# Kernel tuning notes

Hardware: AMD Instinct MI355X
Metric: run time of the kernel (lower is better)

The kernel has to match this reference:

```python
import jax, jax.numpy as jnp
import numpy as np

N_NODES = 100000
N_EDGES = 1600000
IN_DIM = 128
OUT_DIM = 256
EPS = 1e-12


def setup_inputs() -> dict:
    key = jax.random.key(0)
    k1, k2, k3, k4, k5 = jax.random.split(key, 5)
    x = jax.random.normal(k1, (N_NODES, IN_DIM), dtype=jnp.float32)
    edge_index = jax.random.randint(k2, (2, N_EDGES), 0, N_NODES, dtype=jnp.int64)
    edge_weight = jax.random.uniform(k3, (N_EDGES,), dtype=jnp.float32)
    # nn.Linear(in_dim*2, out_dim): weight [out, 2*in], bias [out]
    bound = 1.0 / np.sqrt(2 * IN_DIM)
    W = jax.random.uniform(k4, (OUT_DIM, 2 * IN_DIM), minval=-bound, maxval=bound, dtype=jnp.float32)
    b = jax.random.uniform(k5, (OUT_DIM,), minval=-bound, maxval=bound, dtype=jnp.float32)
    return {"x": x, "edge_index": edge_index, "edge_weight": edge_weight, "W": W, "b": b}


def reference(x, edge_index, edge_weight, W, b):
    src = edge_index[0]
    dst = edge_index[1]
    w = edge_weight.astype(x.dtype)
    # messages: [E, in_dim] = gathered dst features weighted per-edge
    messages = x[dst] * w[:, None]
    agg = jax.ops.segment_sum(messages, src, num_segments=x.shape[0])   # [N, in_dim]
    wsum = jax.ops.segment_sum(w, src, num_segments=x.shape[0])        # [N]
    neigh = agg / jnp.maximum(wsum, EPS)[:, None]
    h = jnp.concatenate([x, neigh], axis=1)                            # [N, 2*in_dim]
    h = h @ W.T + b
    return jax.nn.relu(h)  # dropout is identity in eval / p=0.0
```

## Files before the change

kernel.cpp:

```cpp
#include <hip/hip_runtime.h>
#include <hip/hip_bf16.h>

#define IN_DIM 128
#define OUT_DIM 256
#define KDIM 256
#define EPS 1e-12f
#define CB_NODES 128
#define NB_MAX 1024
#define PART_CHUNK 8192
#define CAP 2560

typedef __attribute__((ext_vector_type(8))) short short8;
typedef __attribute__((ext_vector_type(4))) float f32x4;

static __device__ __forceinline__ unsigned short f2bf(float f) {
  __hip_bfloat16 h = __float2bfloat16(f);
  return *reinterpret_cast<unsigned short*>(&h);
}
static __device__ __forceinline__ unsigned pack2bf(float a, float b) {
  return (unsigned)f2bf(a) | ((unsigned)f2bf(b) << 16);
}
static __device__ __forceinline__ float bf_lo(unsigned v) {
  return __uint_as_float((v & 0xffffu) << 16);
}
static __device__ __forceinline__ float bf_hi(unsigned v) {
  return __uint_as_float(v & 0xffff0000u);
}

__global__ __launch_bounds__(256) void cvt_x(
    const float* __restrict__ x, unsigned short* __restrict__ hb, int N) {
  const int total = N * 32;
  const int stride = gridDim.x * blockDim.x;
  for (int idx = blockIdx.x * blockDim.x + threadIdx.x; idx < total; idx += stride) {
    const int row = idx >> 5;
    const int c4 = (idx & 31) * 4;
    const float4 v = *reinterpret_cast<const float4*>(x + (size_t)row * IN_DIM + c4);
    ushort4 o;
    o.x = f2bf(v.x); o.y = f2bf(v.y); o.z = f2bf(v.z); o.w = f2bf(v.w);
    *reinterpret_cast<ushort4*>(hb + (size_t)row * KDIM + c4) = o;
  }
}

__global__ __launch_bounds__(256) void chist(
    const int* __restrict__ src, int* __restrict__ cnt, int E, int NB) {
  __shared__ int lcnt[NB_MAX];
  for (int i = threadIdx.x; i < NB; i += 256) lcnt[i] = 0;
  __syncthreads();
  const int stride = gridDim.x * blockDim.x;
  for (int e = blockIdx.x * blockDim.x + threadIdx.x; e < E; e += stride)
    atomicAdd(&lcnt[src[e] >> 7], 1);
  __syncthreads();
  for (int i = threadIdx.x; i < NB; i += 256)
    if (lcnt[i]) atomicAdd(&cnt[i], lcnt[i]);
}

__global__ void cscan(const int* __restrict__ cnt, int* __restrict__ bstart,
                      int* __restrict__ gcursor, int NB) {
  const int lane = threadIdx.x;
  int carry = 0;
  for (int base = 0; base < NB; base += 64) {
    const int i = base + lane;
    const int c = (i < NB) ? cnt[i] : 0;
    int incl = c;
    for (int d = 1; d < 64; d <<= 1) {
      int t = __shfl_up(incl, d, 64);
      if (lane >= d) incl += t;
    }
    const int excl = carry + incl - c;
    if (i < NB) { bstart[i] = excl; gcursor[i] = excl; }
    carry += __shfl(incl, 63, 64);
  }
  if (lane == 0) bstart[NB] = carry;
}

__global__ __launch_bounds__(256) void cpartition(
    const int* __restrict__ src, const int* __restrict__ dst,
    const float* __restrict__ ew,
    int* __restrict__ gcursor, int2* __restrict__ recs, int E, int NB) {
  __shared__ int pos[NB_MAX];
  const int c0 = blockIdx.x * PART_CHUNK;
  const int c1 = min(E, c0 + PART_CHUNK);
  for (int i = threadIdx.x; i < NB; i += 256) pos[i] = 0;
  __syncthreads();
  for (int i = c0 + threadIdx.x; i < c1; i += 256)
    atomicAdd(&pos[src[i] >> 7], 1);
  __syncthreads();
  for (int b = threadIdx.x; b < NB; b += 256) {
    const int c = pos[b];
    pos[b] = c ? atomicAdd(&gcursor[b], c) : 0;
  }
  __syncthreads();
  for (int i = c0 + threadIdx.x; i < c1; i += 256) {
    const int s = src[i];
    const int p = atomicAdd(&pos[s >> 7], 1);
    int2 r;
    r.x = dst[i] | ((s & 127) << 17);
    r.y = __float_as_int(ew[i]);
    recs[p] = r;
  }
}

__global__ __launch_bounds__(512) void cagg(
    unsigned short* __restrict__ hb,
    const int* __restrict__ bstart,
    const int2* __restrict__ recs, int N) {
  __shared__ int2 lrec[CAP];
  __shared__ int lstart[CB_NODES + 1];
  __shared__ int lcur[CB_NODES];
  const int tid = threadIdx.x;
  const int lane = tid & 63;
  const int wv = tid >> 6;
  const int blk = blockIdx.x;
  const int e0 = bstart[blk];
  const int e1 = bstart[blk + 1];

  float ax[16], ay[16], ws[16];
#pragma unroll
  for (int n = 0; n < 16; ++n) { ax[n] = 0.f; ay[n] = 0.f; ws[n] = 0.f; }

  for (int base = e0; base < e1; base += CAP) {
    const int m = min(CAP, e1 - base);
    if (tid < CB_NODES) lcur[tid] = 0;
    __syncthreads();
    for (int i = tid; i < m; i += 512)
      atomicAdd(&lcur[recs[base + i].x >> 17], 1);
    __syncthreads();
    if (wv == 0) {
      int carry = 0;
#pragma unroll
      for (int rr = 0; rr < 2; ++rr) {
        const int idx = rr * 64 + lane;
        const int c = lcur[idx];
        int incl = c;
#pragma unroll
        for (int d = 1; d < 64; d <<= 1) {
          int t = __shfl_up(incl, d, 64);
          if (lane >= d) incl += t;
        }
        lstart[idx] = carry + incl - c;
        carry += __shfl(incl, 63, 64);
      }
      if (lane == 0) lstart[CB_NODES] = carry;
    }
    __syncthreads();
    if (tid < CB_NODES) lcur[tid] = lstart[tid];
    __syncthreads();
    for (int i = tid; i < m; i += 512) {
      const int2 r = recs[base + i];
      const int p = atomicAdd(&lcur[r.x >> 17], 1);
      lrec[p] = r;
    }
    __syncthreads();
#pragma unroll
    for (int n = 0; n < 16; ++n) {
      const int rs = lstart[wv * 16 + n];
      const int re = lstart[wv * 16 + n + 1];
      int j = rs;
      for (; j + 4 <= re; j += 4) {
        const int2 r0 = lrec[j + 0];
        const int2 r1 = lrec[j + 1];
        const int2 r2 = lrec[j + 2];
        const int2 r3 = lrec[j + 3];
        const unsigned v0 = *reinterpret_cast<const unsigned*>(
            hb + (size_t)(r0.x & 0x1FFFF) * KDIM + lane * 2);
        const unsigned v1 = *reinterpret_cast<const unsigned*>(
            hb + (size_t)(r1.x & 0x1FFFF) * KDIM + lane * 2);
        const unsigned v2 = *reinterpret_cast<const unsigned*>(
            hb + (size_t)(r2.x & 0x1FFFF) * KDIM + lane * 2);
        const unsigned v3 = *reinterpret_cast<const unsigned*>(
            hb + (size_t)(r3.x & 0x1FFFF) * KDIM + lane * 2);
        const float w0 = __int_as_float(r0.y);
        const float w1 = __int_as_float(r1.y);
        const float w2 = __int_as_float(r2.y);
        const float w3 = __int_as_float(r3.y);
        ax[n] += bf_lo(v0) * w0 + bf_lo(v1) * w1 + bf_lo(v2) * w2 + bf_lo(v3) * w3;
        ay[n] += bf_hi(v0) * w0 + bf_hi(v1) * w1 + bf_hi(v2) * w2 + bf_hi(v3) * w3;
        ws[n] += w0 + w1 + w2 + w3;
      }
      for (; j < re; ++j) {
        const int2 r = lrec[j];
        const unsigned v = *reinterpret_cast<const unsigned*>(
            hb + (size_t)(r.x & 0x1FFFF) * KDIM + lane * 2);
        const float w = __int_as_float(r.y);
        ax[n] += bf_lo(v) * w;
        ay[n] += bf_hi(v) * w;
        ws[n] += w;
      }
    }
    __syncthreads();
  }

#pragma unroll
  for (int n = 0; n < 16; ++n) {
    const int row = wv * 16 + n;
    const int node = blk * CB_NODES + row;
    if (node < N) {
      const float mm = fmaxf(ws[n], EPS);
      *reinterpret_cast<unsigned*>(hb + (size_t)node * KDIM + IN_DIM + lane * 2) =
          pack2bf(ax[n] / mm, ay[n] / mm);
    }
  }
}

__global__ __launch_bounds__(512, 2) void sage_gemm_mfma(
    const unsigned short* __restrict__ hb,
    const float* __restrict__ W,
    const float* __restrict__ bias,
    float* __restrict__ out, int N) {
  __shared__ unsigned short Wl[OUT_DIM * KDIM];
  const int tid = threadIdx.x;
  const int lane = tid & 63;
  const int wv = tid >> 6;

  char* wl = reinterpret_cast<char*>(Wl);
  for (int ch = tid; ch < OUT_DIM * KDIM / 8; ch += 512) {
    const int elem = ch * 8;
    const int j = elem >> 8;
    const int col = elem & 255;
    const float4 w0 = *reinterpret_cast<const float4*>(W + elem);
    const float4 w1 = *reinterpret_cast<const float4*>(W + elem + 4);
    uint4 o;
    o.x = pack2bf(w0.x, w0.y); o.y = pack2bf(w0.z, w0.w);
    o.z = pack2bf(w1.x, w1.y); o.w = pack2bf(w1.z, w1.w);
    const int byte = (j << 9) | ((col * 2) ^ ((j & 7) << 4));
    *reinterpret_cast<uint4*>(wl + byte) = o;
  }

  const int row0 = blockIdx.x * 256 + wv * 32;
  const int kc = (lane >> 4) * 8;
  const unsigned short* arow0 = hb + (size_t)(row0 + (lane & 15)) * KDIM + kc;
  const unsigned short* arow1 = arow0 + 16 * KDIM;
  short8 a0[8], a1[8];
#pragma unroll
  for (int kk = 0; kk < 8; ++kk) {
    a0[kk] = *reinterpret_cast<const short8*>(arow0 + kk * 32);
    a1[kk] = *reinterpret_cast<const short8*>(arow1 + kk * 32);
  }

  __syncthreads();

  f32x4 acc[2][16];
#pragma unroll
  for (int i = 0; i < 2; ++i)
#pragma unroll
    for (int j = 0; j < 16; ++j) acc[i][j] = (f32x4){0.f, 0.f, 0.f, 0.f};

  const int jrow = lane & 15;
  const int kb0 = kc * 2;
#pragma unroll
  for (int kk = 0; kk < 8; ++kk) {
    const int kbyte = kb0 + kk * 64;
#pragma unroll
    for (int ct = 0; ct < 16; ++ct) {
      const int j = ct * 16 + jrow;
      const short8 bf = *reinterpret_cast<const short8*>(
          wl + ((j << 9) | (kbyte ^ ((j & 7) << 4))));
      acc[0][ct] = __builtin_amdgcn_mfma_f32_16x16x32_bf16(a0[kk], bf, acc[0][ct], 0, 0, 0);
      acc[1][ct] = __builtin_amdgcn_mfma_f32_16x16x32_bf16(a1[kk], bf, acc[1][ct], 0, 0, 0);
    }
  }

  const int col = lane & 15;
  const int rquad = (lane >> 4) * 4;
#pragma unroll
  for (int ct = 0; ct < 16; ++ct) {
    const int j = ct * 16 + col;
    const float bj = bias[j];
#pragma unroll
    for (int rt = 0; rt < 2; ++rt) {
      const int rbase = row0 + rt * 16 + rquad;
      const f32x4 a = acc[rt][ct];
#pragma unroll
      for (int r = 0; r < 4; ++r) {
        const int row = rbase + r;
        if (row < N) out[(size_t)row * OUT_DIM + j] = fmaxf(a[r] + bj, 0.f);
      }
    }
  }
}

extern "C" void kernel_launch(void* const* d_in, const int* in_sizes, int n_in,
                              void* d_out, int out_size, void* d_ws, size_t ws_size,
                              hipStream_t stream) {
  const float* x  = (const float*)d_in[0];
  const int*   ei = (const int*)d_in[1];
  const float* ew = (const float*)d_in[2];
  const float* W  = (const float*)d_in[3];
  const float* b  = (const float*)d_in[4];
  float* out = (float*)d_out;

  const int N = in_sizes[0] / IN_DIM;
  const int E = in_sizes[2];
  const int* src = ei;
  const int* dst = ei + E;

  const int gemm_blocks = (N + 255) / 256;
  const int Mpad = gemm_blocks * 256;
  const int NB = (N + CB_NODES - 1) / CB_NODES;

  unsigned short* hb = (unsigned short*)d_ws;
  int2* recs   = (int2*)(hb + (size_t)Mpad * KDIM);
  int* cnt     = (int*)(recs + E);
  int* bstart  = cnt + NB_MAX;
  int* gcursor = bstart + NB_MAX + 1;

  hipMemsetAsync(cnt, 0, NB * sizeof(int), stream);

  cvt_x<<<2048, 256, 0, stream>>>(x, hb, N);
  chist<<<256, 256, 0, stream>>>(src, cnt, E, NB);
  cscan<<<1, 64, 0, stream>>>(cnt, bstart, gcursor, NB);
  cpartition<<<(E + PART_CHUNK - 1) / PART_CHUNK, 256, 0, stream>>>(
      src, dst, ew, gcursor, recs, E, NB);
  cagg<<<NB, 512, 0, stream>>>(hb, bstart, recs, N);
  sage_gemm_mfma<<<gemm_blocks, 512, 0, stream>>>(hb, W, b, out, N);
}
```

Baseline: 401.2 us.

## Split aggregation into single-pass fast path, pre-convert W, retune partition chunks

Aggregation now has two kernels. cagg_fast handles node blocks whose edge count fits in shared memory in a single pass, keeping one node's accumulators live at a time with an 8-way unrolled gather, and declares a higher occupancy target. cagg_slow keeps the old multi-pass path for oversized blocks. W is converted to bf16 once by a separate kernel so the GEMM blocks no longer each convert it. PART_CHUNK is reduced and the histogram grid is doubled for more parallelism, at the cost of one extra kernel launch plus a mostly empty slow-path launch.

```diff
diff --git a/kernel.cpp b/kernel.cpp
--- a/kernel.cpp
+++ b/kernel.cpp
@@ -7,7 +7,7 @@
 #define EPS 1e-12f
 #define CB_NODES 128
 #define NB_MAX 1024
-#define PART_CHUNK 8192
+#define PART_CHUNK 2048
 #define CAP 2560
 
 typedef __attribute__((ext_vector_type(8))) short short8;
@@ -41,6 +41,15 @@
   }
 }
 
+__global__ __launch_bounds__(256) void cvt_w(
+    const float* __restrict__ W, unsigned short* __restrict__ Wb) {
+  const int base = (blockIdx.x * blockDim.x + threadIdx.x) * 4;
+  const float4 v = *reinterpret_cast<const float4*>(W + base);
+  ushort4 o;
+  o.x = f2bf(v.x); o.y = f2bf(v.y); o.z = f2bf(v.z); o.w = f2bf(v.w);
+  *reinterpret_cast<ushort4*>(Wb + base) = o;
+}
+
 __global__ __launch_bounds__(256) void chist(
     const int* __restrict__ src, int* __restrict__ cnt, int E, int NB) {
   __shared__ int lcnt[NB_MAX];
@@ -100,7 +109,7 @@
   }
 }
 
-__global__ __launch_bounds__(512) void cagg(
+__global__ __launch_bounds__(512, 8) void cagg_fast(
     unsigned short* __restrict__ hb,
     const int* __restrict__ bstart,
     const int2* __restrict__ recs, int N) {
@@ -113,6 +122,114 @@
   const int blk = blockIdx.x;
   const int e0 = bstart[blk];
   const int e1 = bstart[blk + 1];
+  const int m = e1 - e0;
+  if (m > CAP) return;
+
+  if (tid < CB_NODES) lcur[tid] = 0;
+  __syncthreads();
+  for (int i = tid; i < m; i += 512)
+    atomicAdd(&lcur[recs[e0 + i].x >> 17], 1);
+  __syncthreads();
+  if (wv == 0) {
+    int carry = 0;
+#pragma unroll
+    for (int rr = 0; rr < 2; ++rr) {
+      const int idx = rr * 64 + lane;
+      const int c = lcur[idx];
+      int incl = c;
+#pragma unroll
+      for (int d = 1; d < 64; d <<= 1) {
+        int t = __shfl_up(incl, d, 64);
+        if (lane >= d) incl += t;
+      }
+      lstart[idx] = carry + incl - c;
+      carry += __shfl(incl, 63, 64);
+    }
+    if (lane == 0) lstart[CB_NODES] = carry;
+  }
+  __syncthreads();
+  if (tid < CB_NODES) lcur[tid] = lstart[tid];
+  __syncthreads();
+  for (int i = tid; i < m; i += 512) {
+    const int2 r = recs[e0 + i];
+    lrec[atomicAdd(&lcur[r.x >> 17], 1)] = r;
+  }
+  __syncthreads();
+
+  for (int n = 0; n < 16; ++n) {
+    const int rs = lstart[wv * 16 + n];
+    const int re = lstart[wv * 16 + n + 1];
+    float ax = 0.f, ay = 0.f, ws = 0.f;
+    int j = rs;
+    for (; j + 8 <= re; j += 8) {
+      const int2 r0 = lrec[j + 0];
+      const int2 r1 = lrec[j + 1];
+      const int2 r2 = lrec[j + 2];
+      const int2 r3 = lrec[j + 3];
+      const int2 r4 = lrec[j + 4];
+      const int2 r5 = lrec[j + 5];
+      const int2 r6 = lrec[j + 6];
+      const int2 r7 = lrec[j + 7];
+      const unsigned v0 = *reinterpret_cast<const unsigned*>(hb + (size_t)(r0.x & 0x1FFFF) * KDIM + lane * 2);
+      const unsigned v1 = *reinterpret_cast<const unsigned*>(hb + (size_t)(r1.x & 0x1FFFF) * KDIM + lane * 2);
+      const unsigned v2 = *reinterpret_cast<const unsigned*>(hb + (size_t)(r2.x & 0x1FFFF) * KDIM + lane * 2);
+      const unsigned v3 = *reinterpret_cast<const unsigned*>(hb + (size_t)(r3.x & 0x1FFFF) * KDIM + lane * 2);
+      const unsigned v4 = *reinterpret_cast<const unsigned*>(hb + (size_t)(r4.x & 0x1FFFF) * KDIM + lane * 2);
+      const unsigned v5 = *reinterpret_cast<const unsigned*>(hb + (size_t)(r5.x & 0x1FFFF) * KDIM + lane * 2);
+      const unsigned v6 = *reinterpret_cast<const unsigned*>(hb + (size_t)(r6.x & 0x1FFFF) * KDIM + lane * 2);
+      const unsigned v7 = *reinterpret_cast<const unsigned*>(hb + (size_t)(r7.x & 0x1FFFF) * KDIM + lane * 2);
+      const float w0 = __int_as_float(r0.y), w1 = __int_as_float(r1.y);
+      const float w2 = __int_as_float(r2.y), w3 = __int_as_float(r3.y);
+      const float w4 = __int_as_float(r4.y), w5 = __int_as_float(r5.y);
+      const float w6 = __int_as_float(r6.y), w7 = __int_as_float(r7.y);
+      ax += bf_lo(v0) * w0 + bf_lo(v1) * w1 + bf_lo(v2) * w2 + bf_lo(v3) * w3
+          + bf_lo(v4) * w4 + bf_lo(v5) * w5 + bf_lo(v6) * w6 + bf_lo(v7) * w7;
+      ay += bf_hi(v0) * w0 + bf_hi(v1) * w1 + bf_hi(v2) * w2 + bf_hi(v3) * w3
+          + bf_hi(v4) * w4 + bf_hi(v5) * w5 + bf_hi(v6) * w6 + bf_hi(v7) * w7;
+      ws += w0 + w1 + w2 + w3 + w4 + w5 + w6 + w7;
+    }
+    for (; j + 2 <= re; j += 2) {
+      const int2 r0 = lrec[j + 0];
+      const int2 r1 = lrec[j + 1];
+      const unsigned v0 = *reinterpret_cast<const unsigned*>(hb + (size_t)(r0.x & 0x1FFFF) * KDIM + lane * 2);
+      const unsigned v1 = *reinterpret_cast<const unsigned*>(hb + (size_t)(r1.x & 0x1FFFF) * KDIM + lane * 2);
+      const float w0 = __int_as_float(r0.y), w1 = __int_as_float(r1.y);
+      ax += bf_lo(v0) * w0 + bf_lo(v1) * w1;
+      ay += bf_hi(v0) * w0 + bf_hi(v1) * w1;
+      ws += w0 + w1;
+    }
+    if (j < re) {
+      const int2 r = lrec[j];
+      const unsigned v = *reinterpret_cast<const unsigned*>(hb + (size_t)(r.x & 0x1FFFF) * KDIM + lane * 2);
+      const float w = __int_as_float(r.y);
+      ax += bf_lo(v) * w;
+      ay += bf_hi(v) * w;
+      ws += w;
+    }
+    const int node = blk * CB_NODES + wv * 16 + n;
+    if (node < N) {
+      const float mm = fmaxf(ws, EPS);
+      *reinterpret_cast<unsigned*>(hb + (size_t)node * KDIM + IN_DIM + lane * 2) =
+          pack2bf(ax / mm, ay / mm);
+    }
+  }
+}
+
+__global__ __launch_bounds__(512) void cagg_slow(
+    unsigned short* __restrict__ hb,
+    const int* __restrict__ bstart,
+    const int2* __restrict__ recs, int N) {
+  const int blk = blockIdx.x;
+  const int e0 = bstart[blk];
+  const int e1 = bstart[blk + 1];
+  if (e1 - e0 <= CAP) return;
+
+  __shared__ int2 lrec[CAP];
+  __shared__ int lstart[CB_NODES + 1];
+  __shared__ int lcur[CB_NODES];
+  const int tid = threadIdx.x;
+  const int lane = tid & 63;
+  const int wv = tid >> 6;
 
   float ax[16], ay[16], ws[16];
 #pragma unroll
@@ -147,37 +264,14 @@
     __syncthreads();
     for (int i = tid; i < m; i += 512) {
       const int2 r = recs[base + i];
-      const int p = atomicAdd(&lcur[r.x >> 17], 1);
-      lrec[p] = r;
+      lrec[atomicAdd(&lcur[r.x >> 17], 1)] = r;
     }
     __syncthreads();
 #pragma unroll
     for (int n = 0; n < 16; ++n) {
       const int rs = lstart[wv * 16 + n];
       const int re = lstart[wv * 16 + n + 1];
-      int j = rs;
-      for (; j + 4 <= re; j += 4) {
-        const int2 r0 = lrec[j + 0];
-        const int2 r1 = lrec[j + 1];
-        const int2 r2 = lrec[j + 2];
-        const int2 r3 = lrec[j + 3];
-        const unsigned v0 = *reinterpret_cast<const unsigned*>(
-            hb + (size_t)(r0.x & 0x1FFFF) * KDIM + lane * 2);
-        const unsigned v1 = *reinterpret_cast<const unsigned*>(
-            hb + (size_t)(r1.x & 0x1FFFF) * KDIM + lane * 2);
-        const unsigned v2 = *reinterpret_cast<const unsigned*>(
-            hb + (size_t)(r2.x & 0x1FFFF) * KDIM + lane * 2);
-        const unsigned v3 = *reinterpret_cast<const unsigned*>(
-            hb + (size_t)(r3.x & 0x1FFFF) * KDIM + lane * 2);
-        const float w0 = __int_as_float(r0.y);
-        const float w1 = __int_as_float(r1.y);
-        const float w2 = __int_as_float(r2.y);
-        const float w3 = __int_as_float(r3.y);
-        ax[n] += bf_lo(v0) * w0 + bf_lo(v1) * w1 + bf_lo(v2) * w2 + bf_lo(v3) * w3;
-        ay[n] += bf_hi(v0) * w0 + bf_hi(v1) * w1 + bf_hi(v2) * w2 + bf_hi(v3) * w3;
-        ws[n] += w0 + w1 + w2 + w3;
-      }
-      for (; j < re; ++j) {
+      for (int j = rs; j < re; ++j) {
         const int2 r = lrec[j];
         const unsigned v = *reinterpret_cast<const unsigned*>(
             hb + (size_t)(r.x & 0x1FFFF) * KDIM + lane * 2);
@@ -192,8 +286,7 @@
 
 #pragma unroll
   for (int n = 0; n < 16; ++n) {
-    const int row = wv * 16 + n;
-    const int node = blk * CB_NODES + row;
+    const int node = blk * CB_NODES + wv * 16 + n;
     if (node < N) {
       const float mm = fmaxf(ws[n], EPS);
       *reinterpret_cast<unsigned*>(hb + (size_t)node * KDIM + IN_DIM + lane * 2) =
@@ -204,7 +297,7 @@
 
 __global__ __launch_bounds__(512, 2) void sage_gemm_mfma(
     const unsigned short* __restrict__ hb,
-    const float* __restrict__ W,
+    const unsigned short* __restrict__ Wb,
     const float* __restrict__ bias,
     float* __restrict__ out, int N) {
   __shared__ unsigned short Wl[OUT_DIM * KDIM];
@@ -213,15 +306,12 @@
   const int wv = tid >> 6;
 
   char* wl = reinterpret_cast<char*>(Wl);
+  const uint4* wbv = reinterpret_cast<const uint4*>(Wb);
   for (int ch = tid; ch < OUT_DIM * KDIM / 8; ch += 512) {
     const int elem = ch * 8;
     const int j = elem >> 8;
     const int col = elem & 255;
-    const float4 w0 = *reinterpret_cast<const float4*>(W + elem);
-    const float4 w1 = *reinterpret_cast<const float4*>(W + elem + 4);
-    uint4 o;
-    o.x = pack2bf(w0.x, w0.y); o.y = pack2bf(w0.z, w0.w);
-    o.z = pack2bf(w1.x, w1.y); o.w = pack2bf(w1.z, w1.w);
+    const uint4 o = wbv[ch];
     const int byte = (j << 9) | ((col * 2) ^ ((j & 7) << 4));
     *reinterpret_cast<uint4*>(wl + byte) = o;
   }
@@ -299,7 +389,8 @@
   const int NB = (N + CB_NODES - 1) / CB_NODES;
 
   unsigned short* hb = (unsigned short*)d_ws;
-  int2* recs   = (int2*)(hb + (size_t)Mpad * KDIM);
+  unsigned short* Wb = hb + (size_t)Mpad * KDIM;
+  int2* recs   = (int2*)(Wb + OUT_DIM * KDIM);
   int* cnt     = (int*)(recs + E);
   int* bstart  = cnt + NB_MAX;
   int* gcursor = bstart + NB_MAX + 1;
@@ -307,10 +398,12 @@
   hipMemsetAsync(cnt, 0, NB * sizeof(int), stream);
 
   cvt_x<<<2048, 256, 0, stream>>>(x, hb, N);
-  chist<<<256, 256, 0, stream>>>(src, cnt, E, NB);
+  cvt_w<<<OUT_DIM * KDIM / 4 / 256, 256, 0, stream>>>(W, Wb);
+  chist<<<512, 256, 0, stream>>>(src, cnt, E, NB);
   cscan<<<1, 64, 0, stream>>>(cnt, bstart, gcursor, NB);
   cpartition<<<(E + PART_CHUNK - 1) / PART_CHUNK, 256, 0, stream>>>(
       src, dst, ew, gcursor, recs, E, NB);
-  cagg<<<NB, 512, 0, stream>>>(hb, bstart, recs, N);
-  sage_gemm_mfma<<<gemm_blocks, 512, 0, stream>>>(hb, W, b, out, N);
-}
+  cagg_fast<<<NB, 512, 0, stream>>>(hb, bstart, recs, N);
+  cagg_slow<<<NB, 512, 0, stream>>>(hb, bstart, recs, N);
+  sage_gemm_mfma<<<gemm_blocks, 512, 0, stream>>>(hb, Wb, b, out, N);
+}
```

Result: faster. 380.6 us (-5.1%).
